# Optimization experiments

Measured on AMD Instinct MI355X. Metric: run time of the kernel, lower is better.

Reference implementation:

```python
import jax, jax.numpy as jnp
import numpy as np

W, B, S, D = 4, 1, 1024, 1024   # simulated world_size, batch, local seq, embed_dim
H, DS, HM = 16, 64, 4            # num_heads, summary_dim, meta_heads


def mha(q, k, v, w_in, b_in, w_out, b_out, nheads):
    """torch nn.MultiheadAttention (batch_first). Returns (out, head-averaged weights)."""
    d = q.shape[-1]
    hd = d // nheads
    wq, wk, wv = jnp.split(w_in, 3, axis=0)
    bq, bk, bv = jnp.split(b_in, 3)
    Bq, Sq, _ = q.shape
    Sk = k.shape[1]
    qh = (q @ wq.T + bq).reshape(Bq, Sq, nheads, hd)
    kh = (k @ wk.T + bk).reshape(Bq, Sk, nheads, hd)
    vh = (v @ wv.T + bv).reshape(Bq, Sk, nheads, hd)
    scores = jnp.einsum('bqhd,bkhd->bhqk', qh, kh) / float(np.sqrt(hd))
    attn = jax.nn.softmax(scores, axis=-1)
    out = jnp.einsum('bhqk,bkhd->bqhd', attn, vh).reshape(Bq, Sq, d)
    return out @ w_out.T + b_out, attn.mean(axis=1)


def attn_stats(attn):
    """attn: (B, S) -> (B, 4) [entropy, gini, max, top5]."""
    ent = -(attn * jnp.log(attn + 1e-8)).sum(-1, keepdims=True)
    s = jnp.sort(attn, axis=-1)
    n = attn.shape[-1]
    idx = jnp.arange(1, n + 1, dtype=attn.dtype)
    gini = 2.0 * (idx * s).sum(-1) / (n * s.sum(-1) + 1e-8) - (n + 1) / n
    mx = attn.max(-1, keepdims=True)
    k = min(5, n)
    top5 = jax.lax.top_k(attn, k)[0].sum(-1, keepdims=True)
    return jnp.concatenate([ent, gini[..., None], mx, top5], axis=-1)


def _forward(x, local_in_w, local_in_b, local_out_w, local_out_b,
             sum_query, sum_in_w, sum_in_b, sum_out_w, sum_out_b,
             pat_w1, pat_b1, pat_w2, pat_b2, comb_w, comb_b,
             meta_in_w, meta_in_b, meta_out_w, meta_out_b,
             route_w1, route_b1, route_w2, route_b2,
             cross_in_w, cross_in_b, cross_out_w, cross_out_b,
             gate_w, gate_b, proj_w, proj_b):
    nW = x.shape[0]

    # 1) local attention per rank: (W,B,S,D)
    local = jax.vmap(lambda xc: mha(xc, xc, xc, local_in_w, local_in_b,
                                    local_out_w, local_out_b, H)[0])(x)

    # 2) chunk summary per rank
    def summarize(lo):
        q = jnp.broadcast_to(sum_query, (lo.shape[0], 1, lo.shape[-1]))
        content, w = mha(q, lo, lo, sum_in_w, sum_in_b, sum_out_w, sum_out_b, H)
        content, w = content[:, 0], w[:, 0]              # (B,D), (B,S)
        pat = attn_stats(w)                               # (B,4)
        pat = jax.nn.relu(pat @ pat_w1.T + pat_b1) @ pat_w2.T + pat_b2
        return jnp.concatenate([content, pat], axis=-1) @ comb_w.T + comb_b

    summaries = jax.vmap(summarize)(local)                # (W,B,DS)
    all_sum = jnp.transpose(summaries, (1, 0, 2))         # (B,W,DS) = all-gather

    # 3) meta attention over chunk summaries -> routing weights
    refined, chunk_attn = mha(all_sum, all_sum, all_sum,
                              meta_in_w, meta_in_b, meta_out_w, meta_out_b, HM)
    logits = (jax.nn.relu(refined @ route_w1.T + route_b1) @ route_w2.T + route_b2)[..., 0]
    routing = jax.nn.softmax(logits, axis=-1)             # (B,W)

    all_chunks = jnp.transpose(local, (1, 0, 2, 3))       # (B,W,S,D) = all-gather

    # 4) selective cross-attention + gated combine, per rank
    def per_rank(r, lo):
        rm = routing * (1.0 - jax.nn.one_hot(r, nW, dtype=routing.dtype))
        rm = rm / (rm.sum(-1, keepdims=True) + 1e-8)
        kv = jnp.einsum('bw,bwsd->bsd', rm, all_chunks)
        cross, _ = mha(lo, kv, kv, cross_in_w, cross_in_b, cross_out_w, cross_out_b, H)
        g = jax.nn.sigmoid(jnp.concatenate([lo, cross], axis=-1) @ gate_w.T + gate_b)
        comb = g * cross + (1.0 - g) * lo
        return comb @ proj_w.T + proj_b

    out = jax.vmap(per_rank)(jnp.arange(nW), local)       # (W,B,S,D)
    return out


def setup_inputs() -> dict:
    key = jax.random.key(0)
    ks = iter(jax.random.split(key, 40))
    p = lambda *shape: jax.random.normal(next(ks), shape, dtype=jnp.float32) * 0.02
    inp = {
        'x': jax.random.normal(next(ks), (W, B, S, D), dtype=jnp.float32),
        'local_in_w': p(3 * D, D), 'local_in_b': p(3 * D),
        'local_out_w': p(D, D), 'local_out_b': p(D),
        'sum_query': p(1, 1, D),
        'sum_in_w': p(3 * D, D), 'sum_in_b': p(3 * D),
        'sum_out_w': p(D, D), 'sum_out_b': p(D),
        'pat_w1': p(DS, 4), 'pat_b1': p(DS),
        'pat_w2': p(DS, DS), 'pat_b2': p(DS),
        'comb_w': p(DS, D + DS), 'comb_b': p(DS),
        'meta_in_w': p(3 * DS, DS), 'meta_in_b': p(3 * DS),
        'meta_out_w': p(DS, DS), 'meta_out_b': p(DS),
        'route_w1': p(DS, DS), 'route_b1': p(DS),
        'route_w2': p(1, DS), 'route_b2': p(1),
        'cross_in_w': p(3 * D, D), 'cross_in_b': p(3 * D),
        'cross_out_w': p(D, D), 'cross_out_b': p(D),
        'gate_w': p(D, 2 * D), 'gate_b': p(D),
        'proj_w': p(D, D), 'proj_b': p(D),
    }
    return inp


def reference(x, local_in_w, local_in_b, local_out_w, local_out_b,
              sum_query, sum_in_w, sum_in_b, sum_out_w, sum_out_b,
              pat_w1, pat_b1, pat_w2, pat_b2, comb_w, comb_b,
              meta_in_w, meta_in_b, meta_out_w, meta_out_b,
              route_w1, route_b1, route_w2, route_b2,
              cross_in_w, cross_in_b, cross_out_w, cross_out_b,
              gate_w, gate_b, proj_w, proj_b):
    return _forward(x, local_in_w, local_in_b, local_out_w, local_out_b,
                    sum_query, sum_in_w, sum_in_b, sum_out_w, sum_out_b,
                    pat_w1, pat_b1, pat_w2, pat_b2, comb_w, comb_b,
                    meta_in_w, meta_in_b, meta_out_w, meta_out_b,
                    route_w1, route_b1, route_w2, route_b2,
                    cross_in_w, cross_in_b, cross_out_w, cross_out_b,
                    gate_w, gate_b, proj_w, proj_b)
```

## Files before the change

kernel.cpp:

```cpp
#include <hip/hip_runtime.h>
#include <hip/hip_bf16.h>
#include <stdint.h>

typedef uint16_t u16;
typedef __attribute__((ext_vector_type(8))) short short8;
typedef __attribute__((ext_vector_type(4))) short short4v;
typedef __attribute__((ext_vector_type(8))) unsigned short ushort8;
typedef __attribute__((ext_vector_type(4))) float f32x4;

#define AS1 __attribute__((address_space(1)))
#define AS3 __attribute__((address_space(3)))

__device__ __forceinline__ float b2f(u16 u){
  union{uint32_t i; float f;} v; v.i=((uint32_t)u)<<16; return v.f;
}
__device__ __forceinline__ u16 f2b(float f){
  union{uint32_t i; float f;} v; v.f=f;
  return (u16)((v.i + 0x7fffu + ((v.i>>16)&1u))>>16);
}
__device__ __forceinline__ u16 f2bf(float f){
  __hip_bfloat16 h = __float2bfloat16(f);
  return *reinterpret_cast<u16*>(&h);
}

struct CvtP { const float* src[8]; u16* dst[8]; long n[8]; };
__global__ void cvt_multi(CvtP p) {
  const int seg = blockIdx.y;
  const long i = ((long)blockIdx.x*256 + threadIdx.x)*8;
  if (i >= p.n[seg]) return;
  const float* in = p.src[seg];
  float4 a = *(const float4*)&in[i];
  float4 b = *(const float4*)&in[i+4];
  ushort8 o;
  o[0]=f2b(a.x); o[1]=f2b(a.y); o[2]=f2b(a.z); o[3]=f2b(a.w);
  o[4]=f2b(b.x); o[5]=f2b(b.y); o[6]=f2b(b.z); o[7]=f2b(b.w);
  *(ushort8*)&p.dst[seg][i] = o;
}

struct GemmP {
  const u16* A; const u16* B; u16* C; const float* bias;
  const u16* B2; u16* C2; const float* bias2;
  const u16* A2; const u16* lr; const u16* cr;
  long lda, ldb, ldc, ldb2, ldc2;
  int K, Nstore, Nstore2, ySplit, act, outf;
  float scale;
};

__global__ __launch_bounds__(512) void gemm_nt(GemmP p) {
  __shared__ __align__(16) u16 lA[2][4096];
  __shared__ __align__(16) u16 lB[2][4096];
  const int t = threadIdx.x;
  const int wave = t >> 6, lane = t & 63;
  int by = blockIdx.y;
  const u16* Bp; u16* Cp; const float* bias; long ldb, ldc; int nst;
  if (by >= p.ySplit) {
    by -= p.ySplit; Bp = p.B2; Cp = p.C2; bias = p.bias2;
    ldb = p.ldb2; ldc = p.ldc2; nst = p.Nstore2;
  } else {
    Bp = p.B; Cp = p.C; bias = p.bias; ldb = p.ldb; ldc = p.ldc; nst = p.Nstore;
  }
  const u16* B = Bp + (long)by * 128 * ldb;
  const int srow = t >> 2, skk = (t & 3) * 8;
  const int wr = wave >> 2, wc = wave & 3;
  const int fr = lane & 15, fk = (lane >> 4) * 8;
  f32x4 acc[4][2] = {};

  const int stepsPerSeg = p.K >> 5;
  const int nseg = p.A2 ? 2 : 1;
  const int total = nseg * stepsPerSeg;
  const u16* A0 = p.A + (long)blockIdx.x * 128 * p.lda;
  const u16* A1 = p.A2 ? (p.A2 + (long)blockIdx.x * 128 * p.lda) : A0;

  auto stage = [&](int s, int b) {
    const int sg = (s >= stepsPerSeg) ? 1 : 0;
    const int k0 = (s - sg*stepsPerSeg) << 5;
    const u16* A = sg ? A1 : A0;
    const u16* Bs = B + (long)sg * p.K;
    __builtin_amdgcn_global_load_lds((const AS1 void*)(A + (long)srow*p.lda + k0 + skk),
                                     (AS3 void*)&lA[b][t*8], 16, 0, 0);
    __builtin_amdgcn_global_load_lds((const AS1 void*)(Bs + (long)srow*ldb + k0 + skk),
                                     (AS3 void*)&lB[b][t*8], 16, 0, 0);
  };

  stage(0, 0);
  asm volatile("s_waitcnt vmcnt(0)" ::: "memory");
  __builtin_amdgcn_s_barrier();

  int cur = 0;
  for (int s = 0; s < total; ++s) {
    if (s + 1 < total) stage(s + 1, cur ^ 1);
    short8 av[4], bv[2];
    #pragma unroll
    for (int mi = 0; mi < 4; ++mi) av[mi] = *(const short8*)&lA[cur][(wr*64 + mi*16 + fr)*32 + fk];
    #pragma unroll
    for (int ni = 0; ni < 2; ++ni) bv[ni] = *(const short8*)&lB[cur][(wc*32 + ni*16 + fr)*32 + fk];
    #pragma unroll
    for (int mi = 0; mi < 4; ++mi)
      #pragma unroll
      for (int ni = 0; ni < 2; ++ni)
        acc[mi][ni] = __builtin_amdgcn_mfma_f32_16x16x32_bf16(av[mi], bv[ni], acc[mi][ni], 0, 0, 0);
    asm volatile("s_waitcnt vmcnt(0)" ::: "memory");
    __builtin_amdgcn_s_barrier();
    cur ^= 1;
  }

  const int rbase = blockIdx.x*128 + wr*64;
  const int cbase = by*128 + wc*32;
  const int rsub = (lane >> 4) * 4;
  #pragma unroll
  for (int ni = 0; ni < 2; ++ni) {
    const int col = cbase + ni*16 + fr;
    if (col >= nst) continue;
    const float bs = bias ? bias[col] : 0.f;
    #pragma unroll
    for (int mi = 0; mi < 4; ++mi) {
      #pragma unroll
      for (int j = 0; j < 4; ++j) {
        float v = acc[mi][ni][j] * p.scale + bs;
        const long idx = (long)(rbase + mi*16 + rsub + j) * ldc + col;
        if (p.act == 2) {
          const float gv = 1.f / (1.f + __expf(-v));
          const float cv = b2f(p.cr[idx]);
          const float lv = b2f(p.lr[idx]);
          Cp[idx] = f2b(gv*cv + (1.f - gv)*lv);
        } else {
          if (p.act == 1) v = 1.f / (1.f + __expf(-v));
          if (p.outf) ((float*)Cp)[idx] = v;
          else        Cp[idx] = f2b(v);
        }
      }
    }
  }
}

struct FlashP {
  const u16 *q, *k, *v; u16* o;
  long ldq, ldkv, ldo;
  long qB, kvB, oB;
};

__global__ __launch_bounds__(256) void flash_k(FlashP p) {
  const int t = threadIdx.x, w4 = t >> 6, lane = t & 63;
  const int bid = blockIdx.x;
  const int qt = bid >> 6;
  const int h  = bid & 15;
  const int wz = (bid >> 4) & 3;
  const int fr = lane & 15, g = lane >> 4, fk = g * 8;
  __shared__ __align__(16) u16 kt[64][72];
  __shared__ __align__(16) u16 vt[64][72];
  __shared__ __align__(16) u16 pl[4][32][72];

  const u16* Q = p.q + (long)wz*p.qB + (long)(qt*128 + w4*32)*p.ldq + h*64;
  const u16* K = p.k + (long)wz*p.kvB + h*64;
  const u16* V = p.v + (long)wz*p.kvB + h*64;

  short8 aq[2][2];
  #pragma unroll
  for (int f = 0; f < 2; ++f) {
    aq[f][0] = *(const short8*)&Q[(long)(f*16 + fr)*p.ldq + fk];
    aq[f][1] = *(const short8*)&Q[(long)(f*16 + fr)*p.ldq + 32 + fk];
  }

  f32x4 acc[2][4] = {};
  float ml[2] = {-3e38f, -3e38f}, ll[2] = {0.f, 0.f};
  const float C = 0.125f * 1.44269504f;

  const int krow = t >> 2, kseg = (t & 3) * 16;
  const int vp = t & 31, vc = (t >> 5) * 8;

  short8 kr0, kr1, vr0, vr1;
  kr0 = *(const short8*)&K[(long)krow*p.ldkv + kseg];
  kr1 = *(const short8*)&K[(long)krow*p.ldkv + kseg + 8];
  vr0 = *(const short8*)&V[(long)(2*vp)*p.ldkv + vc];
  vr1 = *(const short8*)&V[(long)(2*vp + 1)*p.ldkv + vc];

  for (int it = 0; it < 16; ++it) {
    *(short8*)&kt[krow][kseg]     = kr0;
    *(short8*)&kt[krow][kseg + 8] = kr1;
    #pragma unroll
    for (int e = 0; e < 8; ++e) {
      const uint32_t pk = (uint32_t)(uint16_t)vr0[e] | ((uint32_t)(uint16_t)vr1[e] << 16);
      *(uint32_t*)&vt[vc + e][2*vp] = pk;
    }
    __syncthreads();

    if (it + 1 < 16) {
      const int kn = (it + 1) * 64;
      kr0 = *(const short8*)&K[(long)(kn + krow)*p.ldkv + kseg];
      kr1 = *(const short8*)&K[(long)(kn + krow)*p.ldkv + kseg + 8];
      vr0 = *(const short8*)&V[(long)(kn + 2*vp)*p.ldkv + vc];
      vr1 = *(const short8*)&V[(long)(kn + 2*vp + 1)*p.ldkv + vc];
    }

    f32x4 s[2][4] = {};
    __builtin_amdgcn_s_setprio(1);
    #pragma unroll
    for (int ni = 0; ni < 4; ++ni) {
      short8 bk0 = *(const short8*)&kt[ni*16 + fr][fk];
      short8 bk1 = *(const short8*)&kt[ni*16 + fr][32 + fk];
      #pragma unroll
      for (int f = 0; f < 2; ++f) {
        s[f][ni] = __builtin_amdgcn_mfma_f32_16x16x32_bf16(bk0, aq[f][0], s[f][ni], 0, 0, 0);
        s[f][ni] = __builtin_amdgcn_mfma_f32_16x16x32_bf16(bk1, aq[f][1], s[f][ni], 0, 0, 0);
      }
    }
    __builtin_amdgcn_s_setprio(0);

    #pragma unroll
    for (int f = 0; f < 2; ++f) {
      float rm = s[f][0][0];
      #pragma unroll
      for (int ni = 0; ni < 4; ++ni)
        #pragma unroll
        for (int j = 0; j < 4; ++j) rm = fmaxf(rm, s[f][ni][j]);
      rm = fmaxf(rm, __shfl_xor(rm, 16, 64));
      rm = fmaxf(rm, __shfl_xor(rm, 32, 64));
      const float rml = rm * C;

      if (__any(rml > ml[f] + 11.5f)) {
        const float mnl = fmaxf(ml[f], rml);
        const float al = exp2f(ml[f] - mnl);
        const float a0 = __shfl(al, g*4 + 0, 64);
        const float a1 = __shfl(al, g*4 + 1, 64);
        const float a2 = __shfl(al, g*4 + 2, 64);
        const float a3 = __shfl(al, g*4 + 3, 64);
        #pragma unroll
        for (int nv = 0; nv < 4; ++nv) {
          acc[f][nv][0] *= a0; acc[f][nv][1] *= a1;
          acc[f][nv][2] *= a2; acc[f][nv][3] *= a3;
        }
        ll[f] *= al;
        ml[f] = mnl;
      }

      float rs = 0.f;
      u16 pb[4][4];
      #pragma unroll
      for (int ni = 0; ni < 4; ++ni)
        #pragma unroll
        for (int j = 0; j < 4; ++j) {
          const float pv = exp2f(s[f][ni][j]*C - ml[f]);
          rs += pv;
          pb[ni][j] = f2bf(pv);
        }
      rs += __shfl_xor(rs, 16, 64);
      rs += __shfl_xor(rs, 32, 64);
      ll[f] += rs;

      #pragma unroll
      for (int ni = 0; ni < 4; ++ni) {
        short4v pk4;
        pk4[0] = (short)pb[ni][0]; pk4[1] = (short)pb[ni][1];
        pk4[2] = (short)pb[ni][2]; pk4[3] = (short)pb[ni][3];
        *(short4v*)&pl[w4][f*16 + fr][ni*16 + g*4] = pk4;
      }
    }

    __builtin_amdgcn_s_setprio(1);
    #pragma unroll
    for (int ks = 0; ks < 2; ++ks) {
      short8 pa0 = *(const short8*)&pl[w4][fr][ks*32 + fk];
      short8 pa1 = *(const short8*)&pl[w4][16 + fr][ks*32 + fk];
      #pragma unroll
      for (int nv = 0; nv < 4; ++nv) {
        short8 bvv = *(const short8*)&vt[nv*16 + fr][ks*32 + fk];
        acc[0][nv] = __builtin_amdgcn_mfma_f32_16x16x32_bf16(pa0, bvv, acc[0][nv], 0, 0, 0);
        acc[1][nv] = __builtin_amdgcn_mfma_f32_16x16x32_bf16(pa1, bvv, acc[1][nv], 0, 0, 0);
      }
    }
    __builtin_amdgcn_s_setprio(0);
    __syncthreads();
  }

  u16* O = p.o + (long)wz*p.oB + (long)(qt*128 + w4*32)*p.ldo + h*64;
  #pragma unroll
  for (int f = 0; f < 2; ++f) {
    const float l0 = __shfl(ll[f], g*4 + 0, 64);
    const float l1 = __shfl(ll[f], g*4 + 1, 64);
    const float l2 = __shfl(ll[f], g*4 + 2, 64);
    const float l3 = __shfl(ll[f], g*4 + 3, 64);
    const float inv[4] = {1.f/l0, 1.f/l1, 1.f/l2, 1.f/l3};
    #pragma unroll
    for (int j = 0; j < 4; ++j)
      #pragma unroll
      for (int nv = 0; nv < 4; ++nv)
        O[(long)(f*16 + g*4 + j)*p.ldo + nv*16 + fr] = f2bf(acc[f][nv][j] * inv[j]);
  }
}

__global__ void gemv_qs(const float* sq, const float* w, const float* b, float* out) {
  const int t = threadIdx.x, nl = t & 63, kq = t >> 6;
  const int n = blockIdx.x*64 + nl;
  const float* row = w + (long)n * 1024 + kq*256;
  const float* q = sq + kq*256;
  float s = 0.f;
  for (int k = 0; k < 256; k += 4) {
    float4 ww = *(const float4*)&row[k];
    float4 qq = *(const float4*)&q[k];
    s += qq.x*ww.x + qq.y*ww.y + qq.z*ww.z + qq.w*ww.w;
  }
  __shared__ float ps[4][64];
  ps[kq][nl] = s;
  __syncthreads();
  if (t < 64) out[blockIdx.x*64 + t] = ps[0][t]+ps[1][t]+ps[2][t]+ps[3][t] + b[blockIdx.x*64 + t];
}

__global__ void sum_attend(const float* qs, const u16* sumkv, float* content, float* pall) {
  const int h = blockIdx.x, w = blockIdx.y, t = threadIdx.x;
  const int lane = t & 63, wv = t >> 6;
  __shared__ float qsh[64];
  __shared__ float sc[1024];
  __shared__ float rmax[4], rsum[4];
  __shared__ float po[4][64];
  if (t < 64) qsh[t] = qs[h*64 + t];
  __syncthreads();
  const u16* kbase = sumkv + (long)w*2097152 + h*64;
  float e[4];
  float mx = -1e30f;
  #pragma unroll
  for (int j = 0; j < 4; ++j) {
    const int k = j*256 + t;
    const u16* krow = kbase + (long)k * 2048;
    float s = 0.f;
    #pragma unroll
    for (int d = 0; d < 64; d += 8) {
      ushort8 kk = *(const ushort8*)&krow[d];
      #pragma unroll
      for (int q = 0; q < 8; ++q) s += qsh[d+q] * b2f(kk[q]);
    }
    s *= 0.125f;
    e[j] = s;
    mx = fmaxf(mx, s);
  }
  #pragma unroll
  for (int o = 32; o; o >>= 1) mx = fmaxf(mx, __shfl_xor(mx, o, 64));
  if (lane == 0) rmax[wv] = mx;
  __syncthreads();
  mx = fmaxf(fmaxf(rmax[0],rmax[1]), fmaxf(rmax[2],rmax[3]));
  float sum = 0.f;
  #pragma unroll
  for (int j = 0; j < 4; ++j) { e[j] = __expf(e[j]-mx); sum += e[j]; }
  #pragma unroll
  for (int o = 32; o; o >>= 1) sum += __shfl_xor(sum, o, 64);
  if (lane == 0) rsum[wv] = sum;
  __syncthreads();
  const float inv = 1.f / (rsum[0]+rsum[1]+rsum[2]+rsum[3]);
  float* pr = pall + ((long)w*16 + h)*1024;
  #pragma unroll
  for (int j = 0; j < 4; ++j) {
    const int k = j*256 + t;
    const float pn = e[j]*inv;
    sc[k] = pn;
    pr[k] = pn;
  }
  __syncthreads();
  const u16* vbase = sumkv + (long)w*2097152 + 1024 + h*64;
  float o = 0.f;
  const int k0 = wv*256;
  for (int k = k0; k < k0+256; ++k) o += sc[k] * b2f(vbase[(long)k*2048 + lane]);
  po[wv][lane] = o;
  __syncthreads();
  if (t < 64) content[(long)w*1024 + h*64 + t] = po[0][t]+po[1][t]+po[2][t]+po[3][t];
}

__global__ void wavg_k(const float* pall, float* wavg) {
  const int w = blockIdx.y, k = blockIdx.x*256 + threadIdx.x;
  float s = 0.f;
  #pragma unroll
  for (int h = 0; h < 16; ++h) s += pall[((long)w*16 + h)*1024 + k];
  wavg[w*1024 + k] = s * (1.f/16.f);
}

__global__ void contproj_k(const float* content, const float* w_, const float* b, float* out) {
  const int w = blockIdx.y, t = threadIdx.x;
  const int nl = t & 63, kq = t >> 6;
  const int n = blockIdx.x*64 + nl;
  const float* c = content + w*1024 + kq*256;
  const float* row = w_ + (long)n * 1024 + kq*256;
  float s = 0.f;
  for (int k = 0; k < 256; k += 4) {
    float4 ww = *(const float4*)&row[k];
    s += c[k]*ww.x + c[k+1]*ww.y + c[k+2]*ww.z + c[k+3]*ww.w;
  }
  __shared__ float ps[4][64];
  ps[kq][nl] = s;
  __syncthreads();
  if (t < 64) out[w*1024 + blockIdx.x*64 + t] = ps[0][t]+ps[1][t]+ps[2][t]+ps[3][t] + b[blockIdx.x*64 + t];
}

__global__ void stats1_k(const float* wavg, float* part) {
  const int c = blockIdx.x, w = blockIdx.y, t = threadIdx.x;
  __shared__ float a[1024];
  for (int i = t; i < 1024; i += 256) a[i] = wavg[w*1024 + i];
  __syncthreads();
  const int jl = t & 63, iq = t >> 6;
  const int j = c*64 + jl;
  const float aj = a[j];
  int pr = 0;
  const int i0 = iq*256;
  #pragma unroll 8
  for (int i = i0; i < i0+256; ++i) {
    const float ai = a[i];
    pr += (ai < aj) || (ai == aj && i < j);
  }
  __shared__ int prs[4][64];
  prs[iq][jl] = pr;
  __syncthreads();
  if (t < 64) {
    const int rank = 1 + prs[0][jl] + prs[1][jl] + prs[2][jl] + prs[3][jl];
    float ent = -aj * logf(aj + 1e-8f);
    float gnum = (float)rank * aj;
    float ssum = aj;
    float mx = aj;
    float top5 = (rank >= 1020) ? aj : 0.f;
    #pragma unroll
    for (int o = 32; o; o >>= 1) {
      ent += __shfl_xor(ent, o, 64);
      gnum += __shfl_xor(gnum, o, 64);
      ssum += __shfl_xor(ssum, o, 64);
      mx = fmaxf(mx, __shfl_xor(mx, o, 64));
      top5 += __shfl_xor(top5, o, 64);
    }
    if (t == 0) {
      float* pp = part + ((w*16 + c) * 5);
      pp[0]=ent; pp[1]=gnum; pp[2]=ssum; pp[3]=mx; pp[4]=top5;
    }
  }
}

__global__ void stats2_k(const float* part, float* stats) {
  const int w = blockIdx.x, t = threadIdx.x;
  const int c = t & 15, stat = t >> 4;
  float v = 0.f;
  const bool active = stat < 5;
  if (active) v = part[(w*16 + c)*5 + stat];
  #pragma unroll
  for (int o = 8; o; o >>= 1) {
    const float ov = __shfl_xor(v, o, 64);
    v = (stat == 3) ? fmaxf(v, ov) : (v + ov);
  }
  __shared__ float r5[5];
  if (active && c == 0) r5[stat] = v;
  __syncthreads();
  if (t == 0) {
    stats[w*4+0] = r5[0];
    stats[w*4+1] = 2.f*r5[1]/(1024.f*r5[2] + 1e-8f) - 1025.f/1024.f;
    stats[w*4+2] = r5[3];
    stats[w*4+3] = r5[4];
  }
}

__global__ void patsum_k(const float* stats, const float* contprj,
                         const float* pw1, const float* pb1, const float* pw2, const float* pb2,
                         const float* combw, const float* combb, float* summ) {
  const int w = blockIdx.x, t = threadIdx.x;
  const int nl = t & 63, kq = t >> 6;
  __shared__ float p1[64], pat[64];
  __shared__ float ps[4][64];
  __shared__ float ps2[4][64];
  if (t < 64) {
    float s = 0.f;
    #pragma unroll
    for (int k = 0; k < 4; ++k) s += stats[w*4+k] * pw1[t*4+k];
    p1[t] = fmaxf(s + pb1[t], 0.f);
  }
  __syncthreads();
  {
    float s = 0.f;
    const float* rw = pw2 + (long)nl*64 + kq*16;
    const float* pp = p1 + kq*16;
    #pragma unroll
    for (int k = 0; k < 16; ++k) s += pp[k] * rw[k];
    ps[kq][nl] = s;
  }
  __syncthreads();
  if (t < 64) pat[t] = ps[0][t]+ps[1][t]+ps[2][t]+ps[3][t] + pb2[t];
  __syncthreads();
  const float* c = contprj + w*1024;
  const float* row = combw + (long)nl * 1088;
  float s = 0.f;
  const int k0 = kq*272;
  for (int k = k0; k < k0+272; ++k) {
    const float rv = row[k];
    const float cv = (k < 1024) ? c[k] : pat[k-1024];
    s += cv * rv;
  }
  ps2[kq][nl] = s;
  __syncthreads();
  if (t < 64) summ[w*64 + t] = ps2[0][t]+ps2[1][t]+ps2[2][t]+ps2[3][t] + combb[t];
}

__global__ void meta_k(const float* summ, const float* miw, const float* mib,
                       const float* mow, const float* mob, const float* rw1, const float* rb1,
                       const float* rw2, const float* rb2, float* routing) {
  const int t = threadIdx.x;
  __shared__ float qkv[4][192];
  __shared__ float sc[64];
  __shared__ float o[4][64];
  __shared__ float rf[4][64];
  __shared__ float t1[4][64];
  __shared__ float lg[4];
  for (int idx = t; idx < 768; idx += 64) {
    const int w = idx / 192, rrow = idx % 192;
    const float* rw = miw + (long)rrow * 64;
    float s = 0.f;
    for (int k = 0; k < 64; ++k) s += summ[w*64+k] * rw[k];
    qkv[w][rrow] = s + mib[rrow];
  }
  __syncthreads();
  {
    const int h = t >> 4, i = (t >> 2) & 3, j = t & 3;
    float s = 0.f;
    #pragma unroll
    for (int d = 0; d < 16; ++d) s += qkv[i][h*16+d] * qkv[j][64 + h*16+d];
    sc[t] = s * 0.25f;
  }
  __syncthreads();
  if (t < 16) {
    const float a0=sc[t*4], a1=sc[t*4+1], a2=sc[t*4+2], a3=sc[t*4+3];
    const float m = fmaxf(fmaxf(a0,a1), fmaxf(a2,a3));
    const float e0=__expf(a0-m), e1=__expf(a1-m), e2=__expf(a2-m), e3=__expf(a3-m);
    const float s = e0+e1+e2+e3;
    sc[t*4]=e0/s; sc[t*4+1]=e1/s; sc[t*4+2]=e2/s; sc[t*4+3]=e3/s;
  }
  __syncthreads();
  for (int idx = t; idx < 256; idx += 64) {
    const int i = idx >> 6, c = idx & 63, h = c >> 4;
    float s = 0.f;
    #pragma unroll
    for (int j = 0; j < 4; ++j) s += sc[(h*4+i)*4+j] * qkv[j][128 + c];
    o[i][c] = s;
  }
  __syncthreads();
  for (int idx = t; idx < 256; idx += 64) {
    const int i = idx >> 6, n = idx & 63;
    const float* rw = mow + (long)n * 64;
    float s = 0.f;
    for (int k = 0; k < 64; ++k) s += o[i][k] * rw[k];
    rf[i][n] = s + mob[n];
  }
  __syncthreads();
  for (int idx = t; idx < 256; idx += 64) {
    const int i = idx >> 6, n = idx & 63;
    const float* rw = rw1 + (long)n * 64;
    float s = 0.f;
    for (int k = 0; k < 64; ++k) s += rf[i][k] * rw[k];
    t1[i][n] = fmaxf(s + rb1[n], 0.f);
  }
  __syncthreads();
  if (t < 4) {
    float s = 0.f;
    for (int k = 0; k < 64; ++k) s += t1[t][k] * rw2[k];
    lg[t] = s + rb2[0];
  }
  __syncthreads();
  if (t == 0) {
    const float m = fmaxf(fmaxf(lg[0],lg[1]), fmaxf(lg[2],lg[3]));
    float e[4], s = 0.f;
    #pragma unroll
    for (int i = 0; i < 4; ++i) { e[i] = __expf(lg[i]-m); s += e[i]; }
    #pragma unroll
    for (int i = 0; i < 4; ++i) routing[i] = e[i]/s;
  }
}

__global__ void kvr_k(const u16* local, const float* routing, u16* kvr) {
  const int r = blockIdx.y;
  const long e = ((long)blockIdx.x*256 + threadIdx.x) * 8;
  float rm[4]; float s = 0.f;
  #pragma unroll
  for (int w = 0; w < 4; ++w) { rm[w] = (w == r) ? 0.f : routing[w]; s += rm[w]; }
  const float inv = 1.f / (s + 1e-8f);
  ushort8 a0 = *(const ushort8*)&local[e];
  ushort8 a1 = *(const ushort8*)&local[1048576 + e];
  ushort8 a2 = *(const ushort8*)&local[2097152 + e];
  ushort8 a3 = *(const ushort8*)&local[3145728 + e];
  ushort8 out;
  #pragma unroll
  for (int j = 0; j < 8; ++j)
    out[j] = f2b((rm[0]*b2f(a0[j]) + rm[1]*b2f(a1[j]) + rm[2]*b2f(a2[j]) + rm[3]*b2f(a3[j])) * inv);
  *(ushort8*)&kvr[(long)r*1048576 + e] = out;
}

static void gemm1(hipStream_t st, dim3 grid,
                  const u16* A, long lda, const u16* B, long ldb,
                  u16* C, long ldc, const float* bias,
                  int K, int N, float scale, int act, int outf) {
  GemmP p = {};
  p.A=A; p.B=B; p.C=C; p.bias=bias;
  p.lda=lda; p.ldb=ldb; p.ldc=ldc;
  p.K=K; p.Nstore=N; p.ySplit=1<<30; p.act=act; p.outf=outf; p.scale=scale;
  gemm_nt<<<grid, dim3(512), 0, st>>>(p);
}

extern "C" void kernel_launch(void* const* d_in, const int* in_sizes, int n_in,
                              void* d_out, int out_size, void* d_ws, size_t ws_size,
                              hipStream_t stream) {
  (void)in_sizes; (void)n_in; (void)out_size; (void)ws_size;
  const float* x   = (const float*)d_in[0];
  const float* liw = (const float*)d_in[1];
  const float* lib = (const float*)d_in[2];
  const float* low = (const float*)d_in[3];
  const float* lob = (const float*)d_in[4];
  const float* sq  = (const float*)d_in[5];
  const float* siw = (const float*)d_in[6];
  const float* sib = (const float*)d_in[7];
  const float* sow = (const float*)d_in[8];
  const float* sob = (const float*)d_in[9];
  const float* pw1 = (const float*)d_in[10];
  const float* pb1 = (const float*)d_in[11];
  const float* pw2 = (const float*)d_in[12];
  const float* pb2 = (const float*)d_in[13];
  const float* cbw = (const float*)d_in[14];
  const float* cbb = (const float*)d_in[15];
  const float* miw = (const float*)d_in[16];
  const float* mib = (const float*)d_in[17];
  const float* mow = (const float*)d_in[18];
  const float* mob = (const float*)d_in[19];
  const float* rw1 = (const float*)d_in[20];
  const float* rb1 = (const float*)d_in[21];
  const float* rw2 = (const float*)d_in[22];
  const float* rb2 = (const float*)d_in[23];
  const float* ciw = (const float*)d_in[24];
  const float* cib = (const float*)d_in[25];
  const float* cow = (const float*)d_in[26];
  const float* cob = (const float*)d_in[27];
  const float* gw  = (const float*)d_in[28];
  const float* gb  = (const float*)d_in[29];
  const float* pw  = (const float*)d_in[30];
  const float* pb  = (const float*)d_in[31];

  char* ws = (char*)d_ws;
  u16* qkv    = (u16*)(ws + 0);
  u16* aout   = (u16*)(ws + 25165824);
  u16* local  = (u16*)(ws + 33554432);
  u16* scratch= (u16*)(ws + 41943040);
  u16* s2048  = (u16*)(ws + 79691776);
  u16* cq     = (u16*)(ws + 96468992);
  u16* kvr    = (u16*)(ws + 104857600);
  u16* crossb = (u16*)(ws + 113246208);
  char* sf = ws + 121634816;
  float* qs      = (float*)(sf + 0);
  float* pall    = (float*)(sf + 4096);
  float* wavg    = (float*)(sf + 266240);
  float* content = (float*)(sf + 282624);
  float* contprj = (float*)(sf + 299008);
  float* stats   = (float*)(sf + 315392);
  float* summ    = (float*)(sf + 315456);
  float* routing = (float*)(sf + 316480);
  float* part    = (float*)(sf + 316544);
  u16* siwkvb = (u16*)(ws + 122028032);
  u16* lowb   = (u16*)(ws + 126222336);
  u16* ciwb   = (u16*)(ws + 128319488);
  u16* cowb   = (u16*)(ws + 134610944);
  u16* gwb    = (u16*)(ws + 136708096);
  u16* pwb    = (u16*)(ws + 140902400);
  u16* xb   = crossb;
  u16* liwb = scratch;

  CvtP cp;
  cp.src[0]=x;   cp.dst[0]=xb;     cp.n[0]=4194304;
  cp.src[1]=liw; cp.dst[1]=liwb;   cp.n[1]=3145728;
  cp.src[2]=low; cp.dst[2]=lowb;   cp.n[2]=1048576;
  cp.src[3]=siw+1048576; cp.dst[3]=siwkvb; cp.n[3]=2097152;
  cp.src[4]=ciw; cp.dst[4]=ciwb;   cp.n[4]=3145728;
  cp.src[5]=cow; cp.dst[5]=cowb;   cp.n[5]=1048576;
  cp.src[6]=gw;  cp.dst[6]=gwb;    cp.n[6]=2097152;
  cp.src[7]=pw;  cp.dst[7]=pwb;    cp.n[7]=1048576;
  cvt_multi<<<dim3(2048, 8), dim3(256), 0, stream>>>(cp);

  gemm1(stream, dim3(32,24), xb,1024, liwb,1024, qkv,3072, lib, 1024, 3072, 1.f, 0, 0);

  {
    FlashP fp;
    fp.q = qkv; fp.k = qkv + 1024; fp.v = qkv + 2048; fp.o = aout;
    fp.ldq = 3072; fp.ldkv = 3072; fp.ldo = 1024;
    fp.qB = 3145728; fp.kvB = 3145728; fp.oB = 1048576;
    flash_k<<<dim3(512), dim3(256), 0, stream>>>(fp);
  }

  gemm1(stream, dim3(32,8), aout,1024, lowb,1024, local,1024, lob, 1024, 1024, 1.f, 0, 0);

  {
    GemmP p = {};
    p.A = local; p.lda = 1024; p.K = 1024; p.scale = 1.f;
    p.B = ciwb;   p.C = cq;    p.bias = cib;      p.ldb = 1024; p.ldc = 1024; p.Nstore = 1024;
    p.B2 = siwkvb; p.C2 = s2048; p.bias2 = sib+1024; p.ldb2 = 1024; p.ldc2 = 2048; p.Nstore2 = 2048;
    p.ySplit = 8;
    gemm_nt<<<dim3(32,24), dim3(512), 0, stream>>>(p);
  }

  gemv_qs<<<dim3(16), dim3(256), 0, stream>>>(sq, siw, sib, qs);
  sum_attend<<<dim3(16,4), dim3(256), 0, stream>>>(qs, s2048, content, pall);
  wavg_k<<<dim3(4,4), dim3(256), 0, stream>>>(pall, wavg);
  contproj_k<<<dim3(16,4), dim3(256), 0, stream>>>(content, sow, sob, contprj);
  stats1_k<<<dim3(16,4), dim3(256), 0, stream>>>(wavg, part);
  stats2_k<<<dim3(4), dim3(128), 0, stream>>>(part, stats);
  patsum_k<<<dim3(4), dim3(256), 0, stream>>>(stats, contprj, pw1, pb1, pw2, pb2, cbw, cbb, summ);

  meta_k<<<dim3(1), dim3(64), 0, stream>>>(summ, miw, mib, mow, mob, rw1, rb1, rw2, rb2, routing);

  kvr_k<<<dim3(512,4), dim3(256), 0, stream>>>(local, routing, kvr);

  gemm1(stream, dim3(32,16), kvr,1024, ciwb+1048576,1024, s2048,2048, cib+1024, 1024, 2048, 1.f, 0, 0);

  {
    FlashP fp;
    fp.q = cq; fp.k = s2048; fp.v = s2048 + 1024; fp.o = aout;
    fp.ldq = 1024; fp.ldkv = 2048; fp.ldo = 1024;
    fp.qB = 1048576; fp.kvB = 2097152; fp.oB = 1048576;
    flash_k<<<dim3(512), dim3(256), 0, stream>>>(fp);
  }

  gemm1(stream, dim3(32,8), aout,1024, cowb,1024, crossb,1024, cob, 1024, 1024, 1.f, 0, 0);

  {
    GemmP p = {};
    p.A = local; p.A2 = crossb; p.lr = local; p.cr = crossb;
    p.B = gwb; p.C = kvr; p.bias = gb;
    p.lda = 1024; p.ldb = 2048; p.ldc = 1024;
    p.K = 1024; p.Nstore = 1024; p.ySplit = 1<<30; p.act = 2; p.outf = 0; p.scale = 1.f;
    gemm_nt<<<dim3(32,8), dim3(512), 0, stream>>>(p);
  }

  gemm1(stream, dim3(32,8), kvr,1024, pwb,1024, (u16*)d_out,1024, pb, 1024, 1024, 1.f, 0, 1);
}
```

Before: 429.2 us.

## Deepen GEMM LDS pipeline to four buffers with two-stage prefetch

```diff
diff --git a/kernel.cpp b/kernel.cpp
--- a/kernel.cpp
+++ b/kernel.cpp
@@ -47,8 +47,10 @@
 };
 
 __global__ __launch_bounds__(512) void gemm_nt(GemmP p) {
-  __shared__ __align__(16) u16 lA[2][4096];
-  __shared__ __align__(16) u16 lB[2][4096];
+  __shared__ __align__(16) u16 lA0[4096]; __shared__ __align__(16) u16 lB0[4096];
+  __shared__ __align__(16) u16 lA1[4096]; __shared__ __align__(16) u16 lB1[4096];
+  __shared__ __align__(16) u16 lA2[4096]; __shared__ __align__(16) u16 lB2[4096];
+  __shared__ __align__(16) u16 lA3[4096]; __shared__ __align__(16) u16 lB3[4096];
   const int t = threadIdx.x;
   const int wave = t >> 6, lane = t & 63;
   int by = blockIdx.y;
@@ -68,40 +70,51 @@
   const int stepsPerSeg = p.K >> 5;
   const int nseg = p.A2 ? 2 : 1;
   const int total = nseg * stepsPerSeg;
-  const u16* A0 = p.A + (long)blockIdx.x * 128 * p.lda;
-  const u16* A1 = p.A2 ? (p.A2 + (long)blockIdx.x * 128 * p.lda) : A0;
-
-  auto stage = [&](int s, int b) {
+  const u16* A0p = p.A + (long)blockIdx.x * 128 * p.lda;
+  const u16* A1p = p.A2 ? (p.A2 + (long)blockIdx.x * 128 * p.lda) : A0p;
+
+  auto stage = [&](int s, u16* LA, u16* LB) {
     const int sg = (s >= stepsPerSeg) ? 1 : 0;
     const int k0 = (s - sg*stepsPerSeg) << 5;
-    const u16* A = sg ? A1 : A0;
-    const u16* Bs = B + (long)sg * p.K;
-    __builtin_amdgcn_global_load_lds((const AS1 void*)(A + (long)srow*p.lda + k0 + skk),
-                                     (AS3 void*)&lA[b][t*8], 16, 0, 0);
-    __builtin_amdgcn_global_load_lds((const AS1 void*)(Bs + (long)srow*ldb + k0 + skk),
-                                     (AS3 void*)&lB[b][t*8], 16, 0, 0);
+    const u16* Ax = sg ? A1p : A0p;
+    const u16* Bx = B + (long)sg * p.K;
+    __builtin_amdgcn_global_load_lds((const AS1 void*)(Ax + (long)srow*p.lda + k0 + skk),
+                                     (AS3 void*)&LA[t*8], 16, 0, 0);
+    __builtin_amdgcn_global_load_lds((const AS1 void*)(Bx + (long)srow*ldb + k0 + skk),
+                                     (AS3 void*)&LB[t*8], 16, 0, 0);
   };
 
-  stage(0, 0);
-  asm volatile("s_waitcnt vmcnt(0)" ::: "memory");
-  __builtin_amdgcn_s_barrier();
-
-  int cur = 0;
-  for (int s = 0; s < total; ++s) {
-    if (s + 1 < total) stage(s + 1, cur ^ 1);
+  auto step = [&](int s, const u16* LA, const u16* LB, u16* SLA, u16* SLB) {
+    const bool hs = (s + 2 < total);
+    if (hs) stage(s + 2, SLA, SLB);
+    __builtin_amdgcn_sched_barrier(0);
     short8 av[4], bv[2];
     #pragma unroll
-    for (int mi = 0; mi < 4; ++mi) av[mi] = *(const short8*)&lA[cur][(wr*64 + mi*16 + fr)*32 + fk];
-    #pragma unroll
-    for (int ni = 0; ni < 2; ++ni) bv[ni] = *(const short8*)&lB[cur][(wc*32 + ni*16 + fr)*32 + fk];
+    for (int mi = 0; mi < 4; ++mi) av[mi] = *(const short8*)&LA[(wr*64 + mi*16 + fr)*32 + fk];
+    #pragma unroll
+    for (int ni = 0; ni < 2; ++ni) bv[ni] = *(const short8*)&LB[(wc*32 + ni*16 + fr)*32 + fk];
     #pragma unroll
     for (int mi = 0; mi < 4; ++mi)
       #pragma unroll
       for (int ni = 0; ni < 2; ++ni)
         acc[mi][ni] = __builtin_amdgcn_mfma_f32_16x16x32_bf16(av[mi], bv[ni], acc[mi][ni], 0, 0, 0);
-    asm volatile("s_waitcnt vmcnt(0)" ::: "memory");
+    if (hs) asm volatile("s_waitcnt vmcnt(2)" ::: "memory");
+    else    asm volatile("s_waitcnt vmcnt(0)" ::: "memory");
     __builtin_amdgcn_s_barrier();
-    cur ^= 1;
+    __builtin_amdgcn_sched_barrier(0);
+  };
+
+  stage(0, lA0, lB0);
+  stage(1, lA1, lB1);
+  asm volatile("s_waitcnt vmcnt(2)" ::: "memory");
+  __builtin_amdgcn_s_barrier();
+  __builtin_amdgcn_sched_barrier(0);
+
+  for (int s = 0; s < total; s += 4) {
+    step(s + 0, lA0, lB0, lA2, lB2);
+    step(s + 1, lA1, lB1, lA3, lB3);
+    step(s + 2, lA2, lB2, lA0, lB0);
+    step(s + 3, lA3, lB3, lA1, lB1);
   }
 
   const int rbase = blockIdx.x*128 + wr*64;
```

After: 433.1 us. No clear change (+0.9%).
